# Kernel optimization log

Measured on AMD Instinct MI355X. Metric: run time of the kernel, lower is better.

## Reference

```python
import jax, jax.numpy as jnp
import numpy as np

B, S, C, H, R, L = 512, 30, 16, 768, 4, 2
EPS = 1e-5


def setup_inputs() -> dict:
    key = jax.random.key(0)
    ks = jax.random.split(key, 12)
    sc = 1.0 / np.sqrt(H)
    return {
        "slots": jax.random.normal(ks[0], (B, S, H), jnp.float32),
        "cls": jax.random.normal(ks[1], (B, C, H), jnp.float32),
        "a_cur": jax.random.uniform(ks[2], (B, S, C), jnp.float32),
        "a_slot": jax.random.uniform(ks[3], (B, S, S), jnp.float32),
        "a_last": jax.random.uniform(ks[4], (B, S, C), jnp.float32),
        "a_dom": jax.random.uniform(ks[5], (B, S, S), jnp.float32),
        "W_r": jax.random.normal(ks[6], (R, H, H), jnp.float32) * sc,
        "b_r": jax.random.normal(ks[7], (R, H), jnp.float32) * sc,
        "W_s": jax.random.normal(ks[8], (H, H), jnp.float32) * sc,
        "b_s": jax.random.normal(ks[9], (H,), jnp.float32) * sc,
        "W_g": jax.random.normal(ks[10], (2 * H, H), jnp.float32) * sc,
        "b_g": jax.random.normal(ks[11], (H,), jnp.float32) * sc,
    }


def reference(slots, cls, a_cur, a_slot, a_last, a_dom, W_r, b_r, W_s, b_s, W_g, b_g):
    for _ in range(L):
        cls_u = cls @ W_s + b_s            # [B,C,H]
        slots_u = slots @ W_s + b_s        # [B,S,H]
        # all R relation projections of both node sets
        rel_cls = jnp.einsum("bch,rhk->rbck", cls, W_r) + b_r[:, None, None, :]
        rel_slots = jnp.einsum("bsh,rhk->rbsk", slots, W_r) + b_r[:, None, None, :]
        # relation 0: updateSlot <-> current turn
        cls_u = cls_u + jnp.einsum("bsc,bsh->bch", a_cur, rel_slots[0]) / (a_cur.sum(-2)[..., None] + EPS)
        slots_u = slots_u + (a_cur @ rel_cls[0]) / (a_cur.sum(-1, keepdims=True) + EPS)
        # relation 1: updateSlot -> all slots
        slots_u = slots_u + (a_slot @ rel_slots[1]) / (a_slot.sum(-1, keepdims=True) + EPS)
        # relation 2: slot <-> last-update turn
        cls_u = cls_u + jnp.einsum("bsc,bsh->bch", a_last, rel_slots[2]) / (a_last.sum(-2)[..., None] + EPS)
        slots_u = slots_u + (a_last @ rel_cls[2]) / (a_last.sum(-1, keepdims=True) + EPS)
        # relation 3: slot-domain connectivity
        slots_u = slots_u + (a_dom @ rel_slots[3]) / (a_dom.sum(-1, keepdims=True) + EPS)
        # gated relu residual update
        gate_slot = jax.nn.sigmoid(jnp.concatenate([slots_u, slots], -1) @ W_g + b_g)
        gate_cls = jax.nn.sigmoid(jnp.concatenate([cls_u, cls], -1) @ W_g + b_g)
        slots = jax.nn.relu(slots_u) * gate_slot + slots * (1.0 - gate_slot)
        cls = jax.nn.relu(cls_u) * gate_cls + cls * (1.0 - gate_cls)
    return cls[:, 1:, :]  # history CLS states [B, C-1, H]
```

## Files before the change

kernel.cpp:

```cpp
#include <hip/hip_runtime.h>
#include <hip/hip_bf16.h>
#include <cstdint>
#include <cstddef>

typedef __hip_bfloat16 bf16;
typedef __bf16 bf16x8 __attribute__((ext_vector_type(8)));
typedef float f32x4 __attribute__((ext_vector_type(4)));

#define S_D 30
#define C_D 16
#define H_D 768
#define EPS_F 1e-5f

__global__ __launch_bounds__(256) void prep_weights_k(
    const float* __restrict__ W_r, const float* __restrict__ b_r,
    const float* __restrict__ W_s, const float* __restrict__ b_s,
    const float* __restrict__ W_g,
    bf16* __restrict__ Wcat, bf16* __restrict__ Wg, bf16* __restrict__ Wcat2,
    float* __restrict__ bslot, float* __restrict__ bcls)
{
  int id = blockIdx.x*256 + threadIdx.x;
  const int n1 = 768*3840, n2 = 768*1536, n3 = 768*2304;
  if (id < n1) {
    int n = id / 3840, k = id % 3840;
    float w;
    if (k < 768) w = W_s[k*768 + n];
    else { int j = k - 768, kk = j >> 2, seg = j & 3;
           w = W_r[((size_t)seg*768 + kk)*768 + n]; }
    Wcat[id] = __float2bfloat16(w);
  } else if (id < n1 + n2) {
    int j = id - n1; int n = j / 1536, k = j % 1536;
    Wg[j] = __float2bfloat16(W_g[(size_t)k*768 + n]);
  } else if (id < n1 + n2 + n3) {
    int j = id - n1 - n2; int n = j / 2304, k = j % 2304;
    float w;
    if (k < 768) w = W_s[k*768 + n];
    else { int jj = k - 768, kk = jj >> 1, seg = jj & 1;
           w = W_r[((size_t)(seg ? 2 : 0)*768 + kk)*768 + n]; }
    Wcat2[j] = __float2bfloat16(w);
  } else if (id < n1 + n2 + n3 + 768) {
    int n = id - n1 - n2 - n3;
    bslot[n] = b_s[n] + b_r[n] + b_r[768+n] + b_r[2*768+n] + b_r[3*768+n];
    bcls[n]  = b_s[n] + b_r[n] + b_r[2*768+n];
  }
}

__global__ __launch_bounds__(256) void agg1_k(
    const float* __restrict__ slots, const float* __restrict__ cls,
    const float* __restrict__ a_cur, const float* __restrict__ a_slot,
    const float* __restrict__ a_last, const float* __restrict__ a_dom,
    bf16* __restrict__ Gin, bf16* __restrict__ Zs, bf16* __restrict__ Zc,
    int b0, int rsBase)
{
  __shared__ float Lac[30*16], Lal[30*16];
  __shared__ float Las[30*32], Lad[30*32];
  __shared__ float LacT[16*32], LalT[16*32];
  __shared__ float ivr[4*32], ivc[2*16];
  const int lb = blockIdx.x, b = b0 + lb, tid = threadIdx.x;
  const float* ac  = a_cur  + (size_t)b*480;
  const float* as_ = a_slot + (size_t)b*900;
  const float* al  = a_last + (size_t)b*480;
  const float* ad  = a_dom  + (size_t)b*900;

  if (tid < 30) {
    float s1=0, s3=0;
    for (int c=0;c<16;c++){ s1+=ac[tid*16+c]; s3+=al[tid*16+c]; }
    ivr[tid] = 1.f/(s1+EPS_F); ivr[32+tid] = 1.f/(s3+EPS_F);
    float s2=0, s4=0;
    for (int j=0;j<30;j++){ s2+=as_[tid*30+j]; s4+=ad[tid*30+j]; }
    ivr[64+tid] = 1.f/(s2+EPS_F); ivr[96+tid] = 1.f/(s4+EPS_F);
  } else if (tid < 46) {
    int c = tid - 30; float s1=0, s3=0;
    for (int s=0;s<30;s++){ s1+=ac[s*16+c]; s3+=al[s*16+c]; }
    ivc[c] = 1.f/(s1+EPS_F); ivc[16+c] = 1.f/(s3+EPS_F);
  }
  __syncthreads();
  for (int i = tid; i < 480; i += 256) {
    int s = i >> 4;
    Lac[i] = ac[i]*ivr[s];
    Lal[i] = al[i]*ivr[32+s];
  }
  for (int i = tid; i < 960; i += 256) {
    int s = i >> 5, j = i & 31;
    Las[i] = (j < 30) ? as_[s*30+j]*ivr[64+s] : 0.f;
    Lad[i] = (j < 30) ? ad[s*30+j]*ivr[96+s] : 0.f;
  }
  for (int i = tid; i < 512; i += 256) {
    int c = i >> 5, s = i & 31;
    LacT[i] = (s < 30) ? ac[s*16+c]*ivc[c]    : 0.f;
    LalT[i] = (s < 30) ? al[s*16+c]*ivc[16+c] : 0.f;
  }
  __syncthreads();

  float xs[3][32], xc[3][16];
  #pragma unroll
  for (int j = 0; j < 3; ++j) {
    const int h = tid + j*256;
    #pragma unroll
    for (int s = 0; s < 30; ++s) xs[j][s] = slots[((size_t)b*30 + s)*768 + h];
    xs[j][30] = 0.f; xs[j][31] = 0.f;
    #pragma unroll
    for (int c = 0; c < 16; ++c) xc[j][c] = cls[((size_t)b*16 + c)*768 + h];
  }
  #pragma unroll
  for (int j = 0; j < 3; ++j) {
    const int h = tid + j*256;
    bf16* Gs = Gin + ((size_t)lb*30)*1536 + 768 + h;
    #pragma unroll
    for (int s = 0; s < 30; ++s) Gs[(size_t)s*1536] = __float2bfloat16(xs[j][s]);
    bf16* Gc = Gin + ((size_t)(rsBase + lb*16))*1536 + 768 + h;
    #pragma unroll
    for (int c = 0; c < 16; ++c) Gc[(size_t)c*1536] = __float2bfloat16(xc[j][c]);
  }

  #pragma unroll 2
  for (int s = 0; s < 30; ++s) {
    float a1[3] = {}, a2[3] = {}, a3[3] = {}, a4[3] = {};
    #pragma unroll
    for (int q = 0; q < 4; ++q) {
      float4 va = *(const float4*)&Lac[s*16 + q*4];
      float4 vl = *(const float4*)&Lal[s*16 + q*4];
      #pragma unroll
      for (int j = 0; j < 3; ++j) {
        a1[j] += va.x*xc[j][q*4] + va.y*xc[j][q*4+1] + va.z*xc[j][q*4+2] + va.w*xc[j][q*4+3];
        a3[j] += vl.x*xc[j][q*4] + vl.y*xc[j][q*4+1] + vl.z*xc[j][q*4+2] + vl.w*xc[j][q*4+3];
      }
    }
    #pragma unroll
    for (int q = 0; q < 8; ++q) {
      float4 vs = *(const float4*)&Las[s*32 + q*4];
      float4 vd = *(const float4*)&Lad[s*32 + q*4];
      #pragma unroll
      for (int j = 0; j < 3; ++j) {
        a2[j] += vs.x*xs[j][q*4] + vs.y*xs[j][q*4+1] + vs.z*xs[j][q*4+2] + vs.w*xs[j][q*4+3];
        a4[j] += vd.x*xs[j][q*4] + vd.y*xs[j][q*4+1] + vd.z*xs[j][q*4+2] + vd.w*xs[j][q*4+3];
      }
    }
    char* Zrow = (char*)Zs + (((size_t)lb*30 + s)*3072)*2;
    #pragma unroll
    for (int j = 0; j < 3; ++j) {
      const int h = tid + j*256;
      union { bf16 hv[4]; uint2 u; } p;
      p.hv[0] = __float2bfloat16(a1[j]);
      p.hv[1] = __float2bfloat16(a2[j]);
      p.hv[2] = __float2bfloat16(a3[j]);
      p.hv[3] = __float2bfloat16(a4[j]);
      *(uint2*)(Zrow + (size_t)h*8) = p.u;
    }
  }
  #pragma unroll 2
  for (int c = 0; c < 16; ++c) {
    float a1[3] = {}, a3[3] = {};
    #pragma unroll
    for (int q = 0; q < 8; ++q) {
      float4 va = *(const float4*)&LacT[c*32 + q*4];
      float4 vl = *(const float4*)&LalT[c*32 + q*4];
      #pragma unroll
      for (int j = 0; j < 3; ++j) {
        a1[j] += va.x*xs[j][q*4] + va.y*xs[j][q*4+1] + va.z*xs[j][q*4+2] + va.w*xs[j][q*4+3];
        a3[j] += vl.x*xs[j][q*4] + vl.y*xs[j][q*4+1] + vl.z*xs[j][q*4+2] + vl.w*xs[j][q*4+3];
      }
    }
    char* Zrow = (char*)Zc + (((size_t)lb*16 + c)*1536)*2;
    #pragma unroll
    for (int j = 0; j < 3; ++j) {
      const int h = tid + j*256;
      union { bf16 hv[2]; unsigned u; } p;
      p.hv[0] = __float2bfloat16(a1[j]);
      p.hv[1] = __float2bfloat16(a3[j]);
      *(unsigned*)(Zrow + (size_t)h*4) = p.u;
    }
  }
}

__global__ __launch_bounds__(256) void agg2_k(
    const bf16* __restrict__ Xo,
    const float* __restrict__ a_cur, const float* __restrict__ a_last,
    bf16* __restrict__ Zc, int b0)
{
  __shared__ float LacT[16*32], LalT[16*32];
  __shared__ float ivc[2*16];
  const int lb = blockIdx.x, b = b0 + lb, tid = threadIdx.x;
  const float* ac = a_cur  + (size_t)b*480;
  const float* al = a_last + (size_t)b*480;
  if (tid < 16) {
    float s1=0, s3=0;
    for (int s=0;s<30;s++){ s1+=ac[s*16+tid]; s3+=al[s*16+tid]; }
    ivc[tid] = 1.f/(s1+EPS_F); ivc[16+tid] = 1.f/(s3+EPS_F);
  }
  __syncthreads();
  for (int i = tid; i < 512; i += 256) {
    int c = i >> 5, s = i & 31;
    LacT[i] = (s < 30) ? ac[s*16+c]*ivc[c]    : 0.f;
    LalT[i] = (s < 30) ? al[s*16+c]*ivc[16+c] : 0.f;
  }
  __syncthreads();

  float xs[3][32];
  #pragma unroll
  for (int j = 0; j < 3; ++j) {
    const int h = tid + j*256;
    #pragma unroll
    for (int s = 0; s < 30; ++s)
      xs[j][s] = __bfloat162float(Xo[((size_t)(lb*30 + s))*768 + h]);
    xs[j][30] = 0.f; xs[j][31] = 0.f;
  }
  #pragma unroll 2
  for (int c = 0; c < 16; ++c) {
    float a1[3] = {}, a3[3] = {};
    #pragma unroll
    for (int q = 0; q < 8; ++q) {
      float4 va = *(const float4*)&LacT[c*32 + q*4];
      float4 vl = *(const float4*)&LalT[c*32 + q*4];
      #pragma unroll
      for (int j = 0; j < 3; ++j) {
        a1[j] += va.x*xs[j][q*4] + va.y*xs[j][q*4+1] + va.z*xs[j][q*4+2] + va.w*xs[j][q*4+3];
        a3[j] += vl.x*xs[j][q*4] + vl.y*xs[j][q*4+1] + vl.z*xs[j][q*4+2] + vl.w*xs[j][q*4+3];
      }
    }
    char* Zrow = (char*)Zc + (((size_t)lb*16 + c)*1536)*2;
    #pragma unroll
    for (int j = 0; j < 3; ++j) {
      const int h = tid + j*256;
      union { bf16 hv[2]; unsigned u; } p;
      p.hv[0] = __float2bfloat16(a1[j]);
      p.hv[1] = __float2bfloat16(a3[j]);
      *(unsigned*)(Zrow + (size_t)h*4) = p.u;
    }
  }
}

template<int BM, int K, int EPI, int LDA0, int LDA1, int SK, bool DBUF>
__device__ __forceinline__ void gemm_body(
    bf16* __restrict__ As, bf16* __restrict__ Bs, int wg,
    const bf16* __restrict__ A0, const bf16* __restrict__ A1,
    const bf16* __restrict__ Bt, bf16* __restrict__ G,
    bf16* __restrict__ G2, bf16* __restrict__ Xo, float* __restrict__ out,
    const float* __restrict__ bias, const float* __restrict__ bg,
    int b0, int rsB)
{
  constexpr int AM = BM/32;
  const int tid  = threadIdx.x;
  const int lane = tid & 63;
  const int wave = tid >> 6;
  const int wm = wave >> 1, wn = wave & 1;
  const int bm = wg / 6, bn = wg % 6;

  const int swz = (((tid & 7) ^ ((tid >> 3) & 7))) << 3;
  const bf16* Ag0 = A0 + (size_t)(bm*BM + (tid>>3))*LDA0 + swz;
  const bf16* Ag1 = A1 + (size_t)(bm*BM + (tid>>3))*LDA1 + swz;
  const bf16* Bg  = Bt + (size_t)(bn*128 + (tid>>3))*K   + swz;
  const int ldsw = (wave*8)*64;

  f32x4 acc[AM][4] = {};

  auto compute = [&](int buf) {
    const bf16* Asb = As + buf*(BM*64);
    const bf16* Bsb = Bs + buf*8192;
    #pragma unroll
    for (int ks = 0; ks < 64; ks += 32) {
      bf16x8 afv[AM], bfv[4];
      const int sa = ((((ks >> 3) + (lane >> 4)) ^ (lane & 7))) << 3;
      #pragma unroll
      for (int i = 0; i < AM; ++i) {
        int m = wm*(BM/2) + i*16 + (lane & 15);
        afv[i] = *(const bf16x8*)&Asb[m*64 + sa];
      }
      #pragma unroll
      for (int j = 0; j < 4; ++j) {
        int n = wn*64 + j*16 + (lane & 15);
        bfv[j] = *(const bf16x8*)&Bsb[n*64 + sa];
      }
      #pragma unroll
      for (int i = 0; i < AM; ++i)
        #pragma unroll
        for (int j = 0; j < 4; ++j)
          acc[i][j] = __builtin_amdgcn_mfma_f32_16x16x32_bf16(afv[i], bfv[j], acc[i][j], 0, 0, 0);
    }
  };

  if constexpr (!DBUF) {
    const bf16* aP[AM];
    const bf16* bP[4];
    #pragma unroll
    for (int p = 0; p < AM; ++p) aP[p] = Ag0 + (size_t)(p*32)*LDA0;
    #pragma unroll
    for (int p = 0; p < 4; ++p)  bP[p] = Bg + (size_t)(p*32)*K;

    auto step = [&]() {
      #pragma unroll
      for (int p = 0; p < AM; ++p) {
        __builtin_amdgcn_global_load_lds(
          (const __attribute__((address_space(1))) void*)aP[p],
          (__attribute__((address_space(3))) void*)(&As[ldsw + p*2048]), 16, 0, 0);
        aP[p] += 64;
      }
      #pragma unroll
      for (int p = 0; p < 4; ++p) {
        __builtin_amdgcn_global_load_lds(
          (const __attribute__((address_space(1))) void*)bP[p],
          (__attribute__((address_space(3))) void*)(&Bs[ldsw + p*2048]), 16, 0, 0);
        bP[p] += 64;
      }
      __syncthreads();
      compute(0);
      __syncthreads();
    };

    #pragma unroll 1
    for (int t = 0; t < SK/64; ++t) step();
    if constexpr (SK < K) {
      #pragma unroll
      for (int p = 0; p < AM; ++p) aP[p] = Ag1 + (size_t)(p*32)*LDA1;
      #pragma unroll 1
      for (int t = 0; t < (K - SK)/64; ++t) step();
    }
  } else {
    const int NT = K/64;
    auto stage = [&](int buf, int kt) {
      #pragma unroll
      for (int p = 0; p < AM; ++p) {
        const bf16* asrc = (kt < SK) ? (Ag0 + (size_t)(p*32)*LDA0 + kt)
                                     : (Ag1 + (size_t)(p*32)*LDA1 + (kt - SK));
        __builtin_amdgcn_global_load_lds(
          (const __attribute__((address_space(1))) void*)asrc,
          (__attribute__((address_space(3))) void*)(&As[buf*(BM*64) + ldsw + p*2048]), 16, 0, 0);
      }
      #pragma unroll
      for (int p = 0; p < 4; ++p) {
        __builtin_amdgcn_global_load_lds(
          (const __attribute__((address_space(1))) void*)(Bg + (size_t)(p*32)*K + kt),
          (__attribute__((address_space(3))) void*)(&Bs[buf*8192 + ldsw + p*2048]), 16, 0, 0);
      }
    };
    stage(0, 0);
    __syncthreads();
    int cur = 0;
    #pragma unroll 1
    for (int t = 0; t < NT; ++t) {
      if (t + 1 < NT) stage(cur ^ 1, (t + 1)*64);
      compute(cur);
      __syncthreads();
      cur ^= 1;
    }
  }

  const int rbase = bm*BM + wm*(BM/2) + ((lane>>4)<<2);
  const int cbase = bn*128 + wn*64 + (lane & 15);
  #pragma unroll
  for (int i = 0; i < AM; ++i) {
    #pragma unroll
    for (int j = 0; j < 4; ++j) {
      const int col = cbase + j*16;
      #pragma unroll
      for (int r2 = 0; r2 < 4; ++r2) {
        const int row = rbase + i*16 + r2;
        float v = acc[i][j][r2];
        if constexpr (EPI == 0) {
          G[(size_t)row*1536 + col] = __float2bfloat16(v + bias[col]);
        } else if constexpr (EPI == 1) {
          v += bg[col];
          float g = 1.f/(1.f + __expf(-v));
          float u = __bfloat162float(G[(size_t)row*1536 + col]);
          float x = __bfloat162float(G[(size_t)row*1536 + 768 + col]);
          bf16 nv = __float2bfloat16(fmaxf(u, 0.f)*g + x*(1.f - g));
          Xo[(size_t)row*H_D + col] = nv;
          if (row >= rsB)
            G2[((size_t)(row - rsB))*1536 + 768 + col] = nv;
        } else {
          v += bg[col];
          float g = 1.f/(1.f + __expf(-v));
          float u = __bfloat162float(G[(size_t)row*1536 + col]);
          int bb = row >> 4, c = row & 15;
          if (c >= 1) {
            float x = __bfloat162float(Xo[(size_t)row*H_D + col]);
            out[((size_t)(b0 + bb)*15 + (c - 1))*H_D + col] =
                fmaxf(u, 0.f)*g + x*(1.f - g);
          }
        }
      }
    }
  }
}

__device__ __forceinline__ int xcd_swizzle(int bid, int nwg) {
  const int q = nwg >> 3, r = nwg & 7;
  const int xcd = bid & 7, idx = bid >> 3;
  return (xcd < r ? xcd*(q+1) : r*(q+1) + (xcd-r)*q) + idx;
}

template<int BM, int K, int EPI, int LDA0, int LDA1, int SK, bool DBUF>
__global__ __launch_bounds__(256) void gemm_k(
    const bf16* __restrict__ A0, const bf16* __restrict__ A1,
    const bf16* __restrict__ Bt, bf16* __restrict__ G,
    bf16* __restrict__ G2, bf16* __restrict__ Xo, float* __restrict__ out,
    const float* __restrict__ bias, const float* __restrict__ bg,
    int b0, int rsB)
{
  __shared__ __align__(16) bf16 As[(DBUF ? 2 : 1)*BM*64];
  __shared__ __align__(16) bf16 Bs[(DBUF ? 2 : 1)*128*64];
  int wg = xcd_swizzle(blockIdx.x, gridDim.x);
  gemm_body<BM, K, EPI, LDA0, LDA1, SK, DBUF>(As, Bs, wg, A0, A1, Bt, G, G2, Xo,
                                              out, bias, bg, b0, rsB);
}

__global__ __launch_bounds__(256) void proj1_k(
    const bf16* __restrict__ GinSx, const bf16* __restrict__ Zs,
    const bf16* __restrict__ Wcat,  bf16* __restrict__ GS,
    const bf16* __restrict__ GinCx, const bf16* __restrict__ Zc,
    const bf16* __restrict__ Wcat2, bf16* __restrict__ GC,
    const float* __restrict__ bslot, const float* __restrict__ bcls, int nS)
{
  __shared__ __align__(16) bf16 As[64*64];
  __shared__ __align__(16) bf16 Bs[128*64];
  int wg = xcd_swizzle(blockIdx.x, gridDim.x);
  if (wg < nS) {
    gemm_body<64, 3840, 0, 1536, 3072, 768, false>(As, Bs, wg, GinSx, Zs, Wcat, GS,
        nullptr, nullptr, nullptr, bslot, nullptr, 0, 0);
  } else {
    gemm_body<64, 2304, 0, 1536, 1536, 768, false>(As, Bs, wg - nS, GinCx, Zc, Wcat2, GC,
        nullptr, nullptr, nullptr, bcls, nullptr, 0, 0);
  }
}

extern "C" void kernel_launch(void* const* d_in, const int* in_sizes, int n_in,
                              void* d_out, int out_size, void* d_ws, size_t ws_size,
                              hipStream_t stream)
{
  const float* slots  = (const float*)d_in[0];
  const float* cls    = (const float*)d_in[1];
  const float* a_cur  = (const float*)d_in[2];
  const float* a_slot = (const float*)d_in[3];
  const float* a_last = (const float*)d_in[4];
  const float* a_dom  = (const float*)d_in[5];
  const float* W_r    = (const float*)d_in[6];
  const float* b_r    = (const float*)d_in[7];
  const float* W_s    = (const float*)d_in[8];
  const float* b_s    = (const float*)d_in[9];
  const float* W_g    = (const float*)d_in[10];
  const float* b_g    = (const float*)d_in[11];
  float* out = (float*)d_out;

  char* base = (char*)d_ws;
  size_t off = 0;
  auto alloc = [&](size_t bytes) -> void* {
    void* r = base + off;
    off = (off + bytes + 255) & ~(size_t)255;
    return r;
  };

  bf16* Wcat   = (bf16*)alloc((size_t)768*3840*2);
  bf16* Wg     = (bf16*)alloc((size_t)768*1536*2);
  bf16* Wcat2  = (bf16*)alloc((size_t)768*2304*2);
  float* bslot = (float*)alloc(768*4);
  float* bcls  = (float*)alloc(768*4);
  size_t fixedOff = off;

  const size_t perBatch = (size_t)46*1536*2 + (size_t)30*3072*2 + (size_t)16*1536*2;
  int chunkB = 512;
  while (chunkB > 64 && fixedOff + perBatch*(size_t)chunkB + 65536 > ws_size) chunkB -= 64;

  const int rowsA_a = chunkB * (S_D + C_D);
  bf16* Gin = (bf16*)alloc((size_t)rowsA_a*1536*2);
  bf16* Zs  = (bf16*)alloc((size_t)chunkB*S_D*3072*2);
  bf16* Zc  = (bf16*)alloc((size_t)chunkB*C_D*1536*2);

  {
    int tot = 768*3840 + 768*1536 + 768*2304 + 768;
    prep_weights_k<<<(tot+255)/256, 256, 0, stream>>>(W_r, b_r, W_s, b_s, W_g,
                                                      Wcat, Wg, Wcat2, bslot, bcls);
  }

  for (int b0 = 0; b0 < 512; ) {
    const int cb = (512 - b0 < chunkB) ? (512 - b0) : chunkB;
    const int rows_s = cb * S_D;
    const int rows_c = cb * C_D;
    const int rows_a = cb * (S_D + C_D);
    bf16* GinC  = Gin + (size_t)rows_s*1536;
    bf16* Xo    = Zs;
    bf16* XoC   = Xo + (size_t)rows_s*768;
    bf16* GinC2 = Zs + (size_t)rows_a*768;
    const int nS = (rows_s/64)*6, nC = (rows_c/64)*6;

    agg1_k<<<cb, 256, 0, stream>>>(slots, cls, a_cur, a_slot, a_last, a_dom,
                                   Gin, Zs, Zc, b0, rows_s);
    proj1_k<<<nS + nC, 256, 0, stream>>>(Gin + 768, Zs, Wcat, Gin,
                                         GinC + 768, Zc, Wcat2, GinC,
                                         bslot, bcls, nS);
    gemm_k<64, 1536, 1, 1536, 1536, 1536, false><<<(rows_a/64)*6, 256, 0, stream>>>(
        Gin, Gin, Wg, Gin, GinC2, Xo, out, bslot, b_g, b0, rows_s);
    agg2_k<<<cb, 256, 0, stream>>>(Xo, a_cur, a_last, Zc, b0);
    gemm_k<64, 2304, 0, 1536, 1536, 768, true><<<nC, 256, 0, stream>>>(
        GinC2 + 768, Zc, Wcat2, GinC2, nullptr, XoC, out, bcls, b_g, b0, 0);
    gemm_k<64, 1536, 2, 1536, 1536, 1536, true><<<nC, 256, 0, stream>>>(
        GinC2, GinC2, Wg, GinC2, nullptr, XoC, out, bcls, b_g, b0, 0);

    b0 += cb;
  }
}
```

Measured before the change: 507.0 us.

## Double-buffer MODE-0 GEMM path and widen proj1/gate GEMM tiles to 128 rows

Replaces the single-buffer load-sync-compute loop in the MODE-0 GEMM path with a double-buffered pipeline. It prefetches the next K tile through global_load_lds, uses explicit vmcnt waits and s_barrier, and raises wave priority during MFMA compute. It also doubles the M tile from 64 to 128 rows for proj1 and the first gate GEMM, which halves the grid and increases reuse of B tiles. The trade is more LDS per block (up to 64KB) and fewer workgroups, which risks lower occupancy and padding or row-divisibility problems if rows are not multiples of 128.

```diff
diff --git a/kernel.cpp b/kernel.cpp
--- a/kernel.cpp
+++ b/kernel.cpp
@@ -230,7 +230,7 @@
   }
 }
 
-template<int BM, int K, int EPI, int LDA0, int LDA1, int SK, bool DBUF>
+template<int BM, int K, int EPI, int LDA0, int LDA1, int SK, int MODE>
 __device__ __forceinline__ void gemm_body(
     bf16* __restrict__ As, bf16* __restrict__ Bs, int wg,
     const bf16* __restrict__ A0, const bf16* __restrict__ A1,
@@ -253,6 +253,7 @@
   const int ldsw = (wave*8)*64;
 
   f32x4 acc[AM][4] = {};
+  constexpr int NT = K/64;
 
   auto compute = [&](int buf) {
     const bf16* Asb = As + buf*(BM*64);
@@ -279,44 +280,61 @@
     }
   };
 
-  if constexpr (!DBUF) {
+  if constexpr (MODE == 0) {
     const bf16* aP[AM];
     const bf16* bP[4];
     #pragma unroll
     for (int p = 0; p < AM; ++p) aP[p] = Ag0 + (size_t)(p*32)*LDA0;
     #pragma unroll
     for (int p = 0; p < 4; ++p)  bP[p] = Bg + (size_t)(p*32)*K;
-
-    auto step = [&]() {
+    constexpr int NT1 = SK/64;
+
+    auto stageC = [&](int buf) {
       #pragma unroll
       for (int p = 0; p < AM; ++p) {
         __builtin_amdgcn_global_load_lds(
           (const __attribute__((address_space(1))) void*)aP[p],
-          (__attribute__((address_space(3))) void*)(&As[ldsw + p*2048]), 16, 0, 0);
+          (__attribute__((address_space(3))) void*)(&As[buf*(BM*64) + ldsw + p*2048]), 16, 0, 0);
         aP[p] += 64;
       }
       #pragma unroll
       for (int p = 0; p < 4; ++p) {
         __builtin_amdgcn_global_load_lds(
           (const __attribute__((address_space(1))) void*)bP[p],
-          (__attribute__((address_space(3))) void*)(&Bs[ldsw + p*2048]), 16, 0, 0);
+          (__attribute__((address_space(3))) void*)(&Bs[buf*8192 + ldsw + p*2048]), 16, 0, 0);
         bP[p] += 64;
       }
-      __syncthreads();
-      compute(0);
-      __syncthreads();
     };
 
+    stageC(0);
+    int cur = 0;
     #pragma unroll 1
-    for (int t = 0; t < SK/64; ++t) step();
-    if constexpr (SK < K) {
-      #pragma unroll
-      for (int p = 0; p < AM; ++p) aP[p] = Ag1 + (size_t)(p*32)*LDA1;
-      #pragma unroll 1
-      for (int t = 0; t < (K - SK)/64; ++t) step();
+    for (int t = 0; t < NT; ++t) {
+      if (t + 1 < NT) {
+        if constexpr (SK < K) {
+          if (t + 1 == NT1) {
+            #pragma unroll
+            for (int p = 0; p < AM; ++p) aP[p] = Ag1 + (size_t)(p*32)*LDA1;
+          }
+        }
+        stageC(cur ^ 1);
+        if constexpr (AM == 4) asm volatile("s_waitcnt vmcnt(8)" ::: "memory");
+        else                   asm volatile("s_waitcnt vmcnt(6)" ::: "memory");
+      } else {
+        asm volatile("s_waitcnt vmcnt(0)" ::: "memory");
+      }
+      __builtin_amdgcn_sched_barrier(0);
+      __builtin_amdgcn_s_barrier();
+      __builtin_amdgcn_sched_barrier(0);
+      __builtin_amdgcn_s_setprio(1);
+      compute(cur);
+      __builtin_amdgcn_s_setprio(0);
+      __builtin_amdgcn_sched_barrier(0);
+      __builtin_amdgcn_s_barrier();
+      __builtin_amdgcn_sched_barrier(0);
+      cur ^= 1;
     }
   } else {
-    const int NT = K/64;
     auto stage = [&](int buf, int kt) {
       #pragma unroll
       for (int p = 0; p < AM; ++p) {
@@ -389,7 +407,7 @@
   return (xcd < r ? xcd*(q+1) : r*(q+1) + (xcd-r)*q) + idx;
 }
 
-template<int BM, int K, int EPI, int LDA0, int LDA1, int SK, bool DBUF>
+template<int BM, int K, int EPI, int LDA0, int LDA1, int SK, int MODE>
 __global__ __launch_bounds__(256) void gemm_k(
     const bf16* __restrict__ A0, const bf16* __restrict__ A1,
     const bf16* __restrict__ Bt, bf16* __restrict__ G,
@@ -397,10 +415,10 @@
     const float* __restrict__ bias, const float* __restrict__ bg,
     int b0, int rsB)
 {
-  __shared__ __align__(16) bf16 As[(DBUF ? 2 : 1)*BM*64];
-  __shared__ __align__(16) bf16 Bs[(DBUF ? 2 : 1)*128*64];
+  __shared__ __align__(16) bf16 As[2*BM*64];
+  __shared__ __align__(16) bf16 Bs[2*128*64];
   int wg = xcd_swizzle(blockIdx.x, gridDim.x);
-  gemm_body<BM, K, EPI, LDA0, LDA1, SK, DBUF>(As, Bs, wg, A0, A1, Bt, G, G2, Xo,
+  gemm_body<BM, K, EPI, LDA0, LDA1, SK, MODE>(As, Bs, wg, A0, A1, Bt, G, G2, Xo,
                                               out, bias, bg, b0, rsB);
 }
 
@@ -411,14 +429,14 @@
     const bf16* __restrict__ Wcat2, bf16* __restrict__ GC,
     const float* __restrict__ bslot, const float* __restrict__ bcls, int nS)
 {
-  __shared__ __align__(16) bf16 As[64*64];
-  __shared__ __align__(16) bf16 Bs[128*64];
+  __shared__ __align__(16) bf16 As[2*128*64];
+  __shared__ __align__(16) bf16 Bs[2*128*64];
   int wg = xcd_swizzle(blockIdx.x, gridDim.x);
   if (wg < nS) {
-    gemm_body<64, 3840, 0, 1536, 3072, 768, false>(As, Bs, wg, GinSx, Zs, Wcat, GS,
+    gemm_body<128, 3840, 0, 1536, 3072, 768, 0>(As, Bs, wg, GinSx, Zs, Wcat, GS,
         nullptr, nullptr, nullptr, bslot, nullptr, 0, 0);
   } else {
-    gemm_body<64, 2304, 0, 1536, 1536, 768, false>(As, Bs, wg - nS, GinCx, Zc, Wcat2, GC,
+    gemm_body<128, 2304, 0, 1536, 1536, 768, 0>(As, Bs, wg - nS, GinCx, Zc, Wcat2, GC,
         nullptr, nullptr, nullptr, bcls, nullptr, 0, 0);
   }
 }
@@ -480,19 +498,20 @@
     bf16* Xo    = Zs;
     bf16* XoC   = Xo + (size_t)rows_s*768;
     bf16* GinC2 = Zs + (size_t)rows_a*768;
-    const int nS = (rows_s/64)*6, nC = (rows_c/64)*6;
+    const int nS = (rows_s/128)*6, nC = (rows_c/128)*6;
+    const int nC64 = (rows_c/64)*6;
 
     agg1_k<<<cb, 256, 0, stream>>>(slots, cls, a_cur, a_slot, a_last, a_dom,
                                    Gin, Zs, Zc, b0, rows_s);
     proj1_k<<<nS + nC, 256, 0, stream>>>(Gin + 768, Zs, Wcat, Gin,
                                          GinC + 768, Zc, Wcat2, GinC,
                                          bslot, bcls, nS);
-    gemm_k<64, 1536, 1, 1536, 1536, 1536, false><<<(rows_a/64)*6, 256, 0, stream>>>(
+    gemm_k<128, 1536, 1, 1536, 1536, 1536, 0><<<(rows_a/128)*6, 256, 0, stream>>>(
         Gin, Gin, Wg, Gin, GinC2, Xo, out, bslot, b_g, b0, rows_s);
     agg2_k<<<cb, 256, 0, stream>>>(Xo, a_cur, a_last, Zc, b0);
-    gemm_k<64, 2304, 0, 1536, 1536, 768, true><<<nC, 256, 0, stream>>>(
+    gemm_k<64, 2304, 0, 1536, 1536, 768, 1><<<nC64, 256, 0, stream>>>(
         GinC2 + 768, Zc, Wcat2, GinC2, nullptr, XoC, out, bcls, b_g, b0, 0);
-    gemm_k<64, 1536, 2, 1536, 1536, 1536, true><<<nC, 256, 0, stream>>>(
+    gemm_k<64, 1536, 2, 1536, 1536, 1536, 1><<<nC64, 256, 0, stream>>>(
         GinC2, GinC2, Wg, GinC2, nullptr, XoC, out, bcls, b_g, b0, 0);
 
     b0 += cb;
```

Result: slower. 557.8 us (+10.0%).
